# Performance work log

Hardware: AMD Instinct MI355X
Metric: run time of the kernel (lower is better)

The kernel has to match this reference:

```python
import jax, jax.numpy as jnp
import numpy as np


def setup_inputs() -> dict:
    key = jax.random.key(0)
    k1, k2, k3 = jax.random.split(key, 3)
    B, Na, Nb = 64, 8192, 8192
    phases_a = jax.random.normal(k1, (B, Na), dtype=jnp.float32)
    phases_b = jax.random.normal(k2, (B, Nb), dtype=jnp.float32)
    # Binary coupled-pair indicator mask (N_a, N_b)
    coupling_mask = jax.random.randint(k3, (Na, Nb), 0, 2, dtype=jnp.int32)
    return {"phases_a": phases_a, "phases_b": phases_b, "coupling_mask": coupling_mask}


def reference(phases_a, phases_b, coupling_mask):
    """Masked phase-locking value (PLV) between two oscillator banks.

    Mathematically identical to |sum_ij M_ij * exp(i*(a_i - b_j))| / sum(M),
    but computed via trig identities + matmul instead of materializing the
    O(B*Na*Nb) complex tensor:
      real = sum_ij M_ij (cos a_i cos b_j + sin a_i sin b_j)
      imag = sum_ij M_ij (sin a_i cos b_j - cos a_i sin b_j)
    """
    ca, sa = jnp.cos(phases_a), jnp.sin(phases_a)   # (B, Na)
    cb, sb = jnp.cos(phases_b), jnp.sin(phases_b)   # (B, Nb)
    M = coupling_mask.astype(ca.dtype)              # (Na, Nb)
    caM = ca @ M                                    # (B, Nb)
    saM = sa @ M                                    # (B, Nb)
    real = jnp.sum(caM * cb + saM * sb, axis=-1)    # (B,)
    imag = jnp.sum(saM * cb - caM * sb, axis=-1)    # (B,)
    n_pairs = jnp.maximum(M.sum(), jnp.asarray(1.0, ca.dtype))
    return jnp.sqrt(real * real + imag * imag) / n_pairs
```

## Files before the change

### kernel.cpp

```cpp
#include <hip/hip_runtime.h>
#include <hip/hip_bf16.h>

#define NA 8192
#define NB 8192
#define NBATCH 64
#define NC 128
#define BM 128
#define WM 32
#define SPLITK 8
#define KCHUNK (NB / SPLITK)
#define NBLK (SPLITK * NA / BM)

#define XT_BYTES (NC * NB * 2)
#define CTR_OFF  XT_BYTES
#define PBLK_OFF (CTR_OFF + 512)

typedef __bf16 bf16x8 __attribute__((ext_vector_type(8)));
typedef float  f32x4  __attribute__((ext_vector_type(4)));
typedef int    ivec4  __attribute__((ext_vector_type(4)));
typedef unsigned short u16x8 __attribute__((ext_vector_type(8)));

__global__ __launch_bounds__(256) void prep_b_kernel(
    const float* __restrict__ pb, __hip_bfloat16* __restrict__ Xtf,
    int* __restrict__ count)
{
    int tid = blockIdx.x * 256 + threadIdx.x;
    if (tid == 0) *count = 0;

    int b  = tid >> 10;
    int kg = tid & 1023;
    int k  = kg << 3;

    const float4* pp = reinterpret_cast<const float4*>(pb + ((size_t)b << 13) + k);
    float4 v0 = pp[0], v1 = pp[1];
    float ph[8] = {v0.x, v0.y, v0.z, v0.w, v1.x, v1.y, v1.z, v1.w};

    u16x8 cv, sv;
#pragma unroll
    for (int e = 0; e < 8; ++e) {
        float s, c;
        __sincosf(ph[e], &s, &c);
        cv[e] = __builtin_bit_cast(unsigned short, __float2bfloat16(c));
        sv[e] = __builtin_bit_cast(unsigned short, __float2bfloat16(s));
    }

    int kstep = kg >> 2;
    int quad  = kg & 3;
    int t     = b >> 3;
    int m0    = (2 * b) & 15;
    size_t base = (((size_t)(kstep * 8 + t) * 64) + quad * 16 + m0) * 8;
    *reinterpret_cast<u16x8*>(&Xtf[base])     = cv;
    *reinterpret_cast<u16x8*>(&Xtf[base + 8]) = sv;
}

struct Bfrags { bf16x8 v[8]; };

__device__ __forceinline__ Bfrags load_b(const bf16x8* __restrict__ fx) {
    Bfrags b;
#pragma unroll
    for (int t = 0; t < 8; ++t) b.v[t] = fx[t * 64];
    return b;
}

__device__ __forceinline__ bf16x8 conv_a(ivec4 r0, ivec4 r1, int& cnt) {
    unsigned p0 = (unsigned)r0.x | ((unsigned)r0.y << 16);
    unsigned p1 = (unsigned)r0.z | ((unsigned)r0.w << 16);
    unsigned p2 = (unsigned)r1.x | ((unsigned)r1.y << 16);
    unsigned p3 = (unsigned)r1.z | ((unsigned)r1.w << 16);
    cnt += __popc(p0) + __popc(p1) + __popc(p2) + __popc(p3);
    uint4 u;
    u.x = p0 * 0x3F80u;
    u.y = p1 * 0x3F80u;
    u.z = p2 * 0x3F80u;
    u.w = p3 * 0x3F80u;
    return __builtin_bit_cast(bf16x8, u);
}

__global__ __launch_bounds__(256, 2) void gemm_kernel(
    const int* __restrict__ mask, const __hip_bfloat16* __restrict__ Xtfg,
    const float* __restrict__ pa,
    float* __restrict__ Pblk, int* __restrict__ count)
{
    const int tid  = threadIdx.x;
    const int wave = tid >> 6;
    const int lane = tid & 63;
    const int quad = lane >> 4;
    const int m    = lane & 15;
    const int itile = blockIdx.x;
    const int kc    = blockIdx.y;
    const int k0    = kc * KCHUNK;

    const int rowbase = itile * BM + wave * WM;
    const bf16x8* __restrict__ xf = reinterpret_cast<const bf16x8*>(Xtfg);

    f32x4 acc[2][8];
#pragma unroll
    for (int f = 0; f < 2; ++f)
#pragma unroll
        for (int t = 0; t < 8; ++t)
            acc[f][t] = (f32x4){0.f, 0.f, 0.f, 0.f};

    int cnt = 0;

    const int* mrow0 = mask + (size_t)(rowbase + m) * NB + quad * 8;
    const int* mrow1 = mrow0 + (size_t)16 * NB;

    auto load_a = [&](int kkk, ivec4& a00, ivec4& a01, ivec4& a10, ivec4& a11) {
        const ivec4* p0 = reinterpret_cast<const ivec4*>(mrow0 + kkk);
        a00 = __builtin_nontemporal_load(p0);
        a01 = __builtin_nontemporal_load(p0 + 1);
        const ivec4* p1 = reinterpret_cast<const ivec4*>(mrow1 + kkk);
        a10 = __builtin_nontemporal_load(p1);
        a11 = __builtin_nontemporal_load(p1 + 1);
    };

    ivec4 x00, x01, x10, x11;  Bfrags bx;
    ivec4 y00, y01, y10, y11;  Bfrags by;

    load_a(k0, x00, x01, x10, x11);
    bx = load_b(xf + (size_t)(k0 >> 5) * 512 + lane);

    for (int kk = k0; kk < k0 + KCHUNK; kk += 64) {
        load_a(kk + 32, y00, y01, y10, y11);
        by = load_b(xf + (size_t)((kk + 32) >> 5) * 512 + lane);
        {
            bf16x8 a0 = conv_a(x00, x01, cnt);
            bf16x8 a1 = conv_a(x10, x11, cnt);
#pragma unroll
            for (int t = 0; t < 8; ++t) {
                acc[0][t] = __builtin_amdgcn_mfma_f32_16x16x32_bf16(a0, bx.v[t], acc[0][t], 0, 0, 0);
                acc[1][t] = __builtin_amdgcn_mfma_f32_16x16x32_bf16(a1, bx.v[t], acc[1][t], 0, 0, 0);
            }
        }
        const int kn = (kk + 64 < k0 + KCHUNK) ? (kk + 64) : k0;
        load_a(kn, x00, x01, x10, x11);
        bx = load_b(xf + (size_t)(kn >> 5) * 512 + lane);
        {
            bf16x8 a0 = conv_a(y00, y01, cnt);
            bf16x8 a1 = conv_a(y10, y11, cnt);
#pragma unroll
            for (int t = 0; t < 8; ++t) {
                acc[0][t] = __builtin_amdgcn_mfma_f32_16x16x32_bf16(a0, by.v[t], acc[0][t], 0, 0, 0);
                acc[1][t] = __builtin_amdgcn_mfma_f32_16x16x32_bf16(a1, by.v[t], acc[1][t], 0, 0, 0);
            }
        }
    }

    __shared__ float lred[4][64][2];
    const int odd = m & 1;

#pragma unroll
    for (int t = 0; t < 8; ++t) {
        const int b = t * 8 + (m >> 1);
        float rc = 0.f, ic = 0.f;
#pragma unroll
        for (int f = 0; f < 2; ++f)
#pragma unroll
            for (int r = 0; r < 4; ++r) {
                int row = rowbase + f * 16 + quad * 4 + r;
                float ph = pa[(size_t)b * NA + row];
                float sn, cs;
                __sincosf(ph, &sn, &cs);
                float Ax = odd ? sn : cs;
                float Bx = odd ? -cs : sn;
                rc = fmaf(Ax, acc[f][t][r], rc);
                ic = fmaf(Bx, acc[f][t][r], ic);
            }
        rc += __shfl_xor(rc, 1);  ic += __shfl_xor(ic, 1);
        rc += __shfl_xor(rc, 16); ic += __shfl_xor(ic, 16);
        rc += __shfl_xor(rc, 32); ic += __shfl_xor(ic, 32);
        if (quad == 0 && !odd) {
            lred[wave][b][0] = rc;
            lred[wave][b][1] = ic;
        }
    }
    __syncthreads();

    if (tid < 128) {
        float s = lred[0][tid >> 1][tid & 1] + lred[1][tid >> 1][tid & 1]
                + lred[2][tid >> 1][tid & 1] + lred[3][tid >> 1][tid & 1];
        int bid = blockIdx.y * 64 + blockIdx.x;
        Pblk[(size_t)tid * NBLK + bid] = s;
    }

#pragma unroll
    for (int off = 32; off > 0; off >>= 1) cnt += __shfl_down(cnt, off);
    if (lane == 0) atomicAdd(count, cnt);
}

__global__ __launch_bounds__(256) void final_kernel(
    const float* __restrict__ Pblk, const int* __restrict__ count,
    float* __restrict__ out)
{
    const int b = blockIdx.x;
    const int t = threadIdx.x;

    float r = 0.f, im = 0.f;
#pragma unroll
    for (int blk = t; blk < NBLK; blk += 256) {
        r  += Pblk[(size_t)(2 * b)     * NBLK + blk];
        im += Pblk[(size_t)(2 * b + 1) * NBLK + blk];
    }
#pragma unroll
    for (int off = 32; off > 0; off >>= 1) {
        r  += __shfl_down(r, off);
        im += __shfl_down(im, off);
    }

    __shared__ float red[8];
    if ((t & 63) == 0) { red[(t >> 6) * 2] = r; red[(t >> 6) * 2 + 1] = im; }
    __syncthreads();

    if (t == 0) {
        float R = red[0] + red[2] + red[4] + red[6];
        float I = red[1] + red[3] + red[5] + red[7];
        float n = fmaxf((float)(*count), 1.0f);
        out[b] = sqrtf(R * R + I * I) / n;
    }
}

extern "C" void kernel_launch(void* const* d_in, const int* in_sizes, int n_in,
                              void* d_out, int out_size, void* d_ws, size_t ws_size,
                              hipStream_t stream) {
    const float* pa   = (const float*)d_in[0];
    const float* pb   = (const float*)d_in[1];
    const int*   mask = (const int*)d_in[2];
    float* out = (float*)d_out;

    char* ws = (char*)d_ws;
    __hip_bfloat16* Xtf = (__hip_bfloat16*)ws;
    int*   count = (int*)(ws + CTR_OFF);
    float* Pblk  = (float*)(ws + PBLK_OFF);

    prep_b_kernel<<<(NBATCH * NB / 8) / 256, 256, 0, stream>>>(pb, Xtf, count);

    dim3 g(NA / BM, SPLITK);
    gemm_kernel<<<g, 256, 0, stream>>>(mask, Xtf, pa, Pblk, count);

    final_kernel<<<NBATCH, 256, 0, stream>>>(Pblk, count, out);
}
```

Measured before the change: 410.2 us.

## Stage mask and B tiles through LDS with async global-to-LDS double buffering

```diff
diff --git a/kernel.cpp b/kernel.cpp
--- a/kernel.cpp
+++ b/kernel.cpp
@@ -7,8 +7,10 @@
 #define NC 128
 #define BM 128
 #define WM 32
-#define SPLITK 8
+#define SPLITK 16
 #define KCHUNK (NB / SPLITK)
+#define BK 32
+#define NT (KCHUNK / BK)
 #define NBLK (SPLITK * NA / BM)
 
 #define XT_BYTES (NC * NB * 2)
@@ -19,6 +21,12 @@
 typedef float  f32x4  __attribute__((ext_vector_type(4)));
 typedef int    ivec4  __attribute__((ext_vector_type(4)));
 typedef unsigned short u16x8 __attribute__((ext_vector_type(8)));
+
+__device__ __forceinline__ void gload16(const void* g, void* l) {
+    __builtin_amdgcn_global_load_lds(
+        (const __attribute__((address_space(1))) unsigned int*)g,
+        (__attribute__((address_space(3))) unsigned int*)l, 16, 0, 0);
+}
 
 __global__ __launch_bounds__(256) void prep_b_kernel(
     const float* __restrict__ pb, __hip_bfloat16* __restrict__ Xtf,
@@ -29,9 +37,8 @@
 
     int b  = tid >> 10;
     int kg = tid & 1023;
-    int k  = kg << 3;
-
-    const float4* pp = reinterpret_cast<const float4*>(pb + ((size_t)b << 13) + k);
+
+    const float4* pp = reinterpret_cast<const float4*>(pb + ((size_t)b << 13) + (kg << 3));
     float4 v0 = pp[0], v1 = pp[1];
     float ph[8] = {v0.x, v0.y, v0.z, v0.w, v1.x, v1.y, v1.z, v1.w};
 
@@ -51,15 +58,6 @@
     size_t base = (((size_t)(kstep * 8 + t) * 64) + quad * 16 + m0) * 8;
     *reinterpret_cast<u16x8*>(&Xtf[base])     = cv;
     *reinterpret_cast<u16x8*>(&Xtf[base + 8]) = sv;
-}
-
-struct Bfrags { bf16x8 v[8]; };
-
-__device__ __forceinline__ Bfrags load_b(const bf16x8* __restrict__ fx) {
-    Bfrags b;
-#pragma unroll
-    for (int t = 0; t < 8; ++t) b.v[t] = fx[t * 64];
-    return b;
 }
 
 __device__ __forceinline__ bf16x8 conv_a(ivec4 r0, ivec4 r1, int& cnt) {
@@ -76,7 +74,7 @@
     return __builtin_bit_cast(bf16x8, u);
 }
 
-__global__ __launch_bounds__(256, 2) void gemm_kernel(
+__global__ __launch_bounds__(256, 3) void gemm_kernel(
     const int* __restrict__ mask, const __hip_bfloat16* __restrict__ Xtfg,
     const float* __restrict__ pa,
     float* __restrict__ Pblk, int* __restrict__ count)
@@ -89,64 +87,73 @@
     const int itile = blockIdx.x;
     const int kc    = blockIdx.y;
     const int k0    = kc * KCHUNK;
-
-    const int rowbase = itile * BM + wave * WM;
-    const bf16x8* __restrict__ xf = reinterpret_cast<const bf16x8*>(Xtfg);
+    const int rowbase = itile * BM;
+
+    __shared__ int smA[2][BM * BK];
+    __shared__ __hip_bfloat16 smB[2][BK * NC];
+    __shared__ float lred[4][64][2];
+
+    const int r_lo = tid >> 3;
+    const int slot = tid & 7;
+    const int* gA[4];
+#pragma unroll
+    for (int i = 0; i < 4; ++i) {
+        int row = i * 32 + r_lo;
+        int kg  = slot ^ (row & 7);
+        gA[i] = mask + (size_t)(rowbase + row) * NB + k0 + kg * 4;
+    }
+    const char* gB = (const char*)Xtfg + (size_t)(k0 >> 5) * 8192 + (size_t)tid * 16;
+
+    int idxA[2][2];
+#pragma unroll
+    for (int f = 0; f < 2; ++f) {
+        int rA = wave * WM + f * 16 + m;
+#pragma unroll
+        for (int sel = 0; sel < 2; ++sel)
+            idxA[f][sel] = rA * BK + (((quad * 2 + sel) ^ (rA & 7)) << 2);
+    }
 
     f32x4 acc[2][8];
 #pragma unroll
     for (int f = 0; f < 2; ++f)
 #pragma unroll
-        for (int t = 0; t < 8; ++t)
-            acc[f][t] = (f32x4){0.f, 0.f, 0.f, 0.f};
+        for (int u = 0; u < 8; ++u)
+            acc[f][u] = (f32x4){0.f, 0.f, 0.f, 0.f};
 
     int cnt = 0;
 
-    const int* mrow0 = mask + (size_t)(rowbase + m) * NB + quad * 8;
-    const int* mrow1 = mrow0 + (size_t)16 * NB;
-
-    auto load_a = [&](int kkk, ivec4& a00, ivec4& a01, ivec4& a10, ivec4& a11) {
-        const ivec4* p0 = reinterpret_cast<const ivec4*>(mrow0 + kkk);
-        a00 = __builtin_nontemporal_load(p0);
-        a01 = __builtin_nontemporal_load(p0 + 1);
-        const ivec4* p1 = reinterpret_cast<const ivec4*>(mrow1 + kkk);
-        a10 = __builtin_nontemporal_load(p1);
-        a11 = __builtin_nontemporal_load(p1 + 1);
+    auto stage = [&](int buf, int ts) {
+#pragma unroll
+        for (int i = 0; i < 4; ++i)
+            gload16(gA[i] + ts * BK, &smA[buf][i * 1024 + tid * 4]);
+#pragma unroll
+        for (int i = 0; i < 2; ++i)
+            gload16(gB + (size_t)ts * 8192 + i * 4096, &smB[buf][i * 2048 + tid * 8]);
     };
 
-    ivec4 x00, x01, x10, x11;  Bfrags bx;
-    ivec4 y00, y01, y10, y11;  Bfrags by;
-
-    load_a(k0, x00, x01, x10, x11);
-    bx = load_b(xf + (size_t)(k0 >> 5) * 512 + lane);
-
-    for (int kk = k0; kk < k0 + KCHUNK; kk += 64) {
-        load_a(kk + 32, y00, y01, y10, y11);
-        by = load_b(xf + (size_t)((kk + 32) >> 5) * 512 + lane);
-        {
-            bf16x8 a0 = conv_a(x00, x01, cnt);
-            bf16x8 a1 = conv_a(x10, x11, cnt);
-#pragma unroll
-            for (int t = 0; t < 8; ++t) {
-                acc[0][t] = __builtin_amdgcn_mfma_f32_16x16x32_bf16(a0, bx.v[t], acc[0][t], 0, 0, 0);
-                acc[1][t] = __builtin_amdgcn_mfma_f32_16x16x32_bf16(a1, bx.v[t], acc[1][t], 0, 0, 0);
-            }
+    stage(0, 0);
+    int cur = 0;
+    for (int ts = 0; ts < NT; ++ts) {
+        __syncthreads();
+        if (ts + 1 < NT) stage(cur ^ 1, ts + 1);
+
+        ivec4 r0a = *(const ivec4*)&smA[cur][idxA[0][0]];
+        ivec4 r1a = *(const ivec4*)&smA[cur][idxA[0][1]];
+        ivec4 r0b = *(const ivec4*)&smA[cur][idxA[1][0]];
+        ivec4 r1b = *(const ivec4*)&smA[cur][idxA[1][1]];
+        bf16x8 a0 = conv_a(r0a, r1a, cnt);
+        bf16x8 a1 = conv_a(r0b, r1b, cnt);
+
+        const bf16x8* bb = reinterpret_cast<const bf16x8*>(&smB[cur][0]);
+#pragma unroll
+        for (int u = 0; u < 8; ++u) {
+            bf16x8 bf = bb[lane + u * 64];
+            acc[0][u] = __builtin_amdgcn_mfma_f32_16x16x32_bf16(a0, bf, acc[0][u], 0, 0, 0);
+            acc[1][u] = __builtin_amdgcn_mfma_f32_16x16x32_bf16(a1, bf, acc[1][u], 0, 0, 0);
         }
-        const int kn = (kk + 64 < k0 + KCHUNK) ? (kk + 64) : k0;
-        load_a(kn, x00, x01, x10, x11);
-        bx = load_b(xf + (size_t)(kn >> 5) * 512 + lane);
-        {
-            bf16x8 a0 = conv_a(y00, y01, cnt);
-            bf16x8 a1 = conv_a(y10, y11, cnt);
-#pragma unroll
-            for (int t = 0; t < 8; ++t) {
-                acc[0][t] = __builtin_amdgcn_mfma_f32_16x16x32_bf16(a0, by.v[t], acc[0][t], 0, 0, 0);
-                acc[1][t] = __builtin_amdgcn_mfma_f32_16x16x32_bf16(a1, by.v[t], acc[1][t], 0, 0, 0);
-            }
-        }
-    }
-
-    __shared__ float lred[4][64][2];
+        cur ^= 1;
+    }
+
     const int odd = m & 1;
 
 #pragma unroll
@@ -157,7 +164,7 @@
         for (int f = 0; f < 2; ++f)
 #pragma unroll
             for (int r = 0; r < 4; ++r) {
-                int row = rowbase + f * 16 + quad * 4 + r;
+                int row = rowbase + wave * WM + f * 16 + quad * 4 + r;
                 float ph = pa[(size_t)b * NA + row];
                 float sn, cs;
                 __sincosf(ph, &sn, &cs);
```

After: 419.3 us. +2.2%, slower.
